# Optimization experiments

Measured on AMD Instinct MI355X. Metric: run time of the kernel, lower is better.

The kernel has to match this reference:

```python
import jax, jax.numpy as jnp
import numpy as np


def setup_inputs() -> dict:
    key = jax.random.key(0)
    k1, k2 = jax.random.split(key)
    # 8-bit integer pixel values stored as float32 (B, 3, H, W)
    image = jax.random.randint(k1, (8, 3, 1024, 1024), 0, 256).astype(jnp.float32)
    # binary text stream (bits). Present for interface fidelity; the original
    # module's arithmetic discards it (see reference()).
    text_bits = jax.random.randint(k2, (1024,), 0, 2, dtype=jnp.int32)
    return {"image": image, "text_bits": text_bits}


def reference(image, text_bits):
    # Original per-pixel loop:
    #   b = format(p, '08b')            # 8-bit string of pixel p
    #   b = b[:-1] + text_bit           # replace LSB with the text bit
    #   p_new = int(b[:-1], 2)          # <-- slices the text bit back OFF,
    #                                   #     keeping only the top 7 bits
    # So p_new == p >> 1 (integer halving); the text bit never lands in the
    # output. The faithful vectorized form is an elementwise floor-divide by 2.
    return jnp.floor(image * 0.5)
```

## Files before the change

kernel.cpp:

```cpp
#include <hip/hip_runtime.h>


typedef float vfloat4 __attribute__((ext_vector_type(4)));

__global__ __launch_bounds__(256) void stego_halve_stream(const vfloat4* __restrict__ in,
                                                          vfloat4* __restrict__ out,
                                                          int n4) {
    const int stride = gridDim.x * blockDim.x;
    int i = blockIdx.x * blockDim.x + threadIdx.x;
    #pragma unroll 4
    for (; i < n4; i += stride) {
        vfloat4 v = __builtin_nontemporal_load(&in[i]);
        vfloat4 r;
        r.x = floorf(v.x * 0.5f);
        r.y = floorf(v.y * 0.5f);
        r.z = floorf(v.z * 0.5f);
        r.w = floorf(v.w * 0.5f);
        __builtin_nontemporal_store(r, &out[i]);
    }
}

__global__ __launch_bounds__(256) void stego_halve_tail(const float* __restrict__ in,
                                                        float* __restrict__ out,
                                                        int start, int n) {
    int i = start + blockIdx.x * blockDim.x + threadIdx.x;
    if (i < n) {
        out[i] = floorf(in[i] * 0.5f);
    }
}

extern "C" void kernel_launch(void* const* d_in, const int* in_sizes, int n_in,
                              void* d_out, int out_size, void* d_ws, size_t ws_size,
                              hipStream_t stream) {
    const float* image = (const float*)d_in[0];
    float* out = (float*)d_out;
    int n = in_sizes[0];

    int n4 = n / 4;
    int tail_start = n4 * 4;

    if (n4 > 0) {
        const int block = 256;
        int threads_needed = (n4 + 3) / 4;
        int grid = (threads_needed + block - 1) / block;
        stego_halve_stream<<<grid, block, 0, stream>>>((const vfloat4*)image,
                                                       (vfloat4*)out, n4);
    }
    if (tail_start < n) {
        int rem = n - tail_start;
        const int block = 256;
        int grid = (rem + block - 1) / block;
        stego_halve_tail<<<grid, block, 0, stream>>>(image, out, tail_start, n);
    }
}
```

Before: 170.3 us.

## Merge tail into a capped-grid stream kernel with batched plain vector loads

Fuses the vector-stream and scalar-tail kernels into one launch. The grid is capped at 2048 blocks with a grid-stride loop that issues four independent float4 loads before storing. The nontemporal load/store builtins are replaced with ordinary accesses. The aim is more memory-level parallelism per thread and less launch overhead, at the cost of losing the cache-bypass hints and relying on a fixed block cap for this 25M-element stream.

```diff
diff --git a/kernel.cpp b/kernel.cpp
--- a/kernel.cpp
+++ b/kernel.cpp
@@ -3,29 +3,40 @@
 
 typedef float vfloat4 __attribute__((ext_vector_type(4)));
 
-__global__ __launch_bounds__(256) void stego_halve_stream(const vfloat4* __restrict__ in,
-                                                          vfloat4* __restrict__ out,
-                                                          int n4) {
-    const int stride = gridDim.x * blockDim.x;
-    int i = blockIdx.x * blockDim.x + threadIdx.x;
-    #pragma unroll 4
-    for (; i < n4; i += stride) {
-        vfloat4 v = __builtin_nontemporal_load(&in[i]);
-        vfloat4 r;
-        r.x = floorf(v.x * 0.5f);
-        r.y = floorf(v.y * 0.5f);
-        r.z = floorf(v.z * 0.5f);
-        r.w = floorf(v.w * 0.5f);
-        __builtin_nontemporal_store(r, &out[i]);
-    }
+__device__ __forceinline__ vfloat4 halve_floor4(vfloat4 v) {
+    vfloat4 r;
+    r.x = floorf(v.x * 0.5f);
+    r.y = floorf(v.y * 0.5f);
+    r.z = floorf(v.z * 0.5f);
+    r.w = floorf(v.w * 0.5f);
+    return r;
 }
 
-__global__ __launch_bounds__(256) void stego_halve_tail(const float* __restrict__ in,
-                                                        float* __restrict__ out,
-                                                        int start, int n) {
-    int i = start + blockIdx.x * blockDim.x + threadIdx.x;
-    if (i < n) {
-        out[i] = floorf(in[i] * 0.5f);
+__global__ __launch_bounds__(256) void stego_halve(const float* __restrict__ in,
+                                                   float* __restrict__ out,
+                                                   int n4, int n) {
+    const int stride = gridDim.x * blockDim.x;
+    const int tid = blockIdx.x * blockDim.x + threadIdx.x;
+    const vfloat4* __restrict__ in4 = (const vfloat4*)in;
+    vfloat4* __restrict__ out4 = (vfloat4*)out;
+
+    int i = tid;
+    for (; i + 3 * stride < n4; i += 4 * stride) {
+        vfloat4 v0 = in4[i];
+        vfloat4 v1 = in4[i + stride];
+        vfloat4 v2 = in4[i + 2 * stride];
+        vfloat4 v3 = in4[i + 3 * stride];
+        out4[i]              = halve_floor4(v0);
+        out4[i + stride]     = halve_floor4(v1);
+        out4[i + 2 * stride] = halve_floor4(v2);
+        out4[i + 3 * stride] = halve_floor4(v3);
+    }
+    for (; i < n4; i += stride) {
+        out4[i] = halve_floor4(in4[i]);
+    }
+    int t = n4 * 4 + tid;
+    if (t < n) {
+        out[t] = floorf(in[t] * 0.5f);
     }
 }
 
@@ -37,19 +48,13 @@
     int n = in_sizes[0];
 
     int n4 = n / 4;
-    int tail_start = n4 * 4;
 
-    if (n4 > 0) {
-        const int block = 256;
-        int threads_needed = (n4 + 3) / 4;
-        int grid = (threads_needed + block - 1) / block;
-        stego_halve_stream<<<grid, block, 0, stream>>>((const vfloat4*)image,
-                                                       (vfloat4*)out, n4);
-    }
-    if (tail_start < n) {
-        int rem = n - tail_start;
-        const int block = 256;
-        int grid = (rem + block - 1) / block;
-        stego_halve_tail<<<grid, block, 0, stream>>>(image, out, tail_start, n);
-    }
+    const int block = 256;
+    long long threads_needed = ((long long)n4 + 3) / 4;
+    if (threads_needed < 1) threads_needed = 1;
+    int grid = (int)((threads_needed + block - 1) / block);
+    if (grid > 2048) grid = 2048;
+    if (grid < 1) grid = 1;
+
+    stego_halve<<<grid, block, 0, stream>>>(image, out, n4, n);
 }
```

Result: slower. 183.7 us (+7.9%).
